# Optimization experiments

Measured on AMD Instinct MI355X. Metric: run time of the kernel, lower is better.

Reference implementation:

```python
import jax, jax.numpy as jnp
import numpy as np

EMBED_DIM = 768
NUM_HEADS = 12
HEAD_DIM = EMBED_DIM // NUM_HEADS
SCALING = HEAD_DIM ** -0.5
B, S = 2, 2048


def setup_inputs() -> dict:
    key = jax.random.key(0)
    k1, k2, k3 = jax.random.split(key, 3)
    x_q = jax.random.normal(k1, (B, S, EMBED_DIM), dtype=jnp.float32)
    # xavier-uniform-ish scaling for weights
    lim_qkv = (6.0 / (EMBED_DIM + 3 * EMBED_DIM)) ** 0.5
    lim_out = (6.0 / (2 * EMBED_DIM)) ** 0.5
    w_qkv = jax.random.uniform(k2, (3 * EMBED_DIM, EMBED_DIM), jnp.float32, -lim_qkv, lim_qkv)
    b_qkv = jnp.zeros((3 * EMBED_DIM,), jnp.float32)
    w_out = jax.random.uniform(k3, (EMBED_DIM, EMBED_DIM), jnp.float32, -lim_out, lim_out)
    b_out = jnp.zeros((EMBED_DIM,), jnp.float32)
    return {"x_q": x_q, "w_qkv": w_qkv, "b_qkv": b_qkv, "w_out": w_out, "b_out": b_out}


def reference(x_q, w_qkv, b_qkv, w_out, b_out):
    b_sz, s_len, _ = x_q.shape
    # qkv projection: (B,S,3E) -> (B,S,3,H,hd) -> split
    qkv = x_q @ w_qkv.T + b_qkv
    qkv = qkv.reshape(b_sz, s_len, 3, NUM_HEADS, HEAD_DIM)
    q = qkv[:, :, 0].transpose(0, 2, 1, 3) * SCALING  # (B,H,S,hd)
    k = qkv[:, :, 1].transpose(0, 2, 1, 3)
    v = qkv[:, :, 2].transpose(0, 2, 1, 3)
    attn = jnp.einsum("bhsd,bhtd->bhst", q, k)  # (B,H,S,S)
    attn = jax.nn.softmax(attn.astype(jnp.float32), axis=-1).astype(attn.dtype)
    out = jnp.einsum("bhst,bhtd->bhsd", attn, v)  # (B,H,S,hd)
    out = out.transpose(0, 2, 1, 3).reshape(b_sz, s_len, EMBED_DIM)
    return out @ w_out.T + b_out
```

## Files before the change

### kernel.cpp

```cpp
#include <hip/hip_runtime.h>
#include <hip/hip_bf16.h>
#include <math.h>

typedef unsigned short u16;
typedef unsigned int u32;
typedef __attribute__((ext_vector_type(8))) short bf16x8;
typedef __attribute__((ext_vector_type(4))) short bf16x4;
typedef __attribute__((ext_vector_type(4))) float f32x4;

#define EMBED 768
#define NHEADS 12
#define HDIM 64
#define NBATCH 2
#define SEQ 2048
#define NTOK 4096
#define QKV_N 2304
#define BHTOT 24
#define QSCALE 0.18033688011112042f

__device__ __forceinline__ u16 f2b(float f) {
    __hip_bfloat16 h = __float2bfloat16(f);
    return __builtin_bit_cast(u16, h);
}
__device__ __forceinline__ u32 pk2(float a, float b) {
    return (u32)f2b(a) | ((u32)f2b(b) << 16);
}
__device__ __forceinline__ f32x4 mfma32(bf16x8 a, bf16x8 b, f32x4 c) {
    return __builtin_amdgcn_mfma_f32_16x16x32_bf16(a, b, c, 0, 0, 0);
}
#if __has_builtin(__builtin_amdgcn_mfma_f32_16x16x16_bf16)
__device__ __forceinline__ f32x4 mfma16(bf16x4 a, bf16x4 b, f32x4 c) {
    return __builtin_amdgcn_mfma_f32_16x16x16_bf16(a, b, c, 0, 0, 0);
}
#else
__device__ __forceinline__ f32x4 mfma16(bf16x4 a, bf16x4 b, f32x4 c) {
    return __builtin_amdgcn_mfma_f32_16x16x16bf16_1k(a, b, c, 0, 0, 0);
}
#endif

__device__ __forceinline__ float exp2_hw(float x) {
#if __has_builtin(__builtin_amdgcn_exp2f)
    return __builtin_amdgcn_exp2f(x);
#else
    float r;
    asm("v_exp_f32 %0, %1" : "=v"(r) : "v"(x));
    return r;
#endif
}

__device__ __forceinline__ void async16(const u16* g, u16* l) {
    __builtin_amdgcn_global_load_lds(
        (const __attribute__((address_space(1))) unsigned int*)g,
        (__attribute__((address_space(3))) unsigned int*)l,
        16, 0, 0);
}

__global__ __launch_bounds__(256)
void cast_kernel(const float* __restrict__ s0, u16* __restrict__ d0, int n0,
                 const float* __restrict__ s1, u16* __restrict__ d1, int n1,
                 const float* __restrict__ s2, u16* __restrict__ d2, int n2)
{
    int idx = (blockIdx.x * 256 + threadIdx.x) * 4;
    const float* s; u16* d; int i;
    if (idx < n0)            { s = s0; d = d0; i = idx; }
    else if (idx < n0 + n1)  { s = s1; d = d1; i = idx - n0; }
    else                     { s = s2; d = d2; i = idx - n0 - n1; if (i >= n2) return; }
    float4 v = *(const float4*)&s[i];
    ushort4 o;
    o.x = f2b(v.x); o.y = f2b(v.y); o.z = f2b(v.z); o.w = f2b(v.w);
    *(ushort4*)&d[i] = o;
}

__global__ __launch_bounds__(256, 3)
void qkv_gemm(const u16* __restrict__ A, const u16* __restrict__ W,
              const float* __restrict__ bias,
              u16* __restrict__ Qb, u16* __restrict__ Kb, u16* __restrict__ VT)
{
    __shared__ __align__(16) u16 smem[24576];
    const int m0 = blockIdx.x * 128;
    const int n0 = blockIdx.y * 128;
    const int tid = threadIdx.x;
    const int w = tid >> 6, l = tid & 63;
    const int c = l & 15, q = l >> 4;
    const int wm = (w >> 1) * 64, wn = (w & 1) * 64;
    const int sr = l >> 2;
    const int gch2 = (l & 3) ^ ((l >> 3) & 3);
    const int NK = EMBED / 32;

#define QSTAGE(KT, BS) {                                                      \
    int k0 = (KT) * 32;                                                       \
    _Pragma("unroll")                                                         \
    for (int j = 0; j < 2; ++j) {                                             \
        int row = j * 64 + w * 16 + sr;                                       \
        int seg = (BS) * 8192 + (j * 64 + w * 16) * 32;                       \
        async16(&A[(size_t)(m0 + row) * EMBED + k0 + gch2 * 8],               \
                &smem[seg + l * 8]);                                          \
        async16(&W[(size_t)(n0 + row) * EMBED + k0 + gch2 * 8],               \
                &smem[seg + 4096 + l * 8]);                                   \
    }                                                                         \
}

    f32x4 acc[4][4] = {};

#define QBODY(KT, BC, BS) {                                                   \
    if ((KT) + 1 < NK) asm volatile("s_waitcnt vmcnt(4)" ::: "memory");       \
    else               asm volatile("s_waitcnt vmcnt(0)" ::: "memory");       \
    __builtin_amdgcn_s_barrier();                                             \
    if ((KT) + 2 < NK) QSTAGE((KT) + 2, BS);                                  \
    const u16* Ab = &smem[(BC) * 8192];                                       \
    const u16* Bb = &smem[(BC) * 8192 + 4096];                                \
    const int cs = (q ^ ((c >> 1) & 3)) << 3;                                 \
    bf16x8 af[4], bfr[4];                                                     \
    _Pragma("unroll")                                                         \
    for (int i = 0; i < 4; ++i)                                               \
        af[i] = *(const bf16x8*)&Ab[(wm + i * 16 + c) * 32 + cs];             \
    _Pragma("unroll")                                                         \
    for (int j = 0; j < 4; ++j)                                               \
        bfr[j] = *(const bf16x8*)&Bb[(wn + j * 16 + c) * 32 + cs];            \
    __builtin_amdgcn_s_setprio(1);                                            \
    _Pragma("unroll")                                                         \
    for (int i = 0; i < 4; ++i)                                               \
        _Pragma("unroll")                                                     \
        for (int j = 0; j < 4; ++j)                                           \
            acc[i][j] = mfma32(af[i], bfr[j], acc[i][j]);                     \
    __builtin_amdgcn_s_setprio(0);                                            \
}

    QSTAGE(0, 0);
    QSTAGE(1, 1);

    for (int kt0 = 0; kt0 < NK; kt0 += 3) {
        QBODY(kt0 + 0, 0, 2);
        QBODY(kt0 + 1, 1, 0);
        QBODY(kt0 + 2, 2, 1);
    }
#undef QSTAGE
#undef QBODY

    const int p = n0 / EMBED;
    const int ncol0 = n0 + wn;
    const int h = (ncol0 % EMBED) / HDIM;
    const int mrow0 = m0 + wm;
    const int b = mrow0 >> 11;
    const int s0 = mrow0 & (SEQ - 1);

    if (p < 2) {
        u16* dst = (p == 0) ? Qb : Kb;
        const float mul = (p == 0) ? QSCALE : 1.0f;
        #pragma unroll
        for (int j = 0; j < 4; ++j) {
            int n = ncol0 + j * 16 + c;
            int d = j * 16 + c;
            float bval = bias[n];
            #pragma unroll
            for (int i = 0; i < 4; ++i) {
                #pragma unroll
                for (int r = 0; r < 4; ++r) {
                    int s = s0 + i * 16 + q * 4 + r;
                    float v = (acc[i][j][r] + bval) * mul;
                    dst[(((size_t)(b * NHEADS + h)) * SEQ + s) * HDIM + d] = f2b(v);
                }
            }
        }
    } else {
        __syncthreads();
        u16* T = smem + w * (64 * 72);
        #pragma unroll
        for (int j = 0; j < 4; ++j) {
            int n = ncol0 + j * 16 + c;
            float bval = bias[n];
            #pragma unroll
            for (int i = 0; i < 4; ++i) {
                uint2 pr;
                pr.x = pk2(acc[i][j][0] + bval, acc[i][j][1] + bval);
                pr.y = pk2(acc[i][j][2] + bval, acc[i][j][3] + bval);
                *(uint2*)&T[(j * 16 + c) * 72 + i * 16 + q * 4] = pr;
            }
        }
        const size_t vtbase = ((size_t)(b * NHEADS + h)) * HDIM * SEQ + s0;
        #pragma unroll
        for (int ii = 0; ii < 8; ++ii) {
            int d = (l >> 3) + 8 * ii;
            int sch = (l & 7) * 8;
            uint4 vv = *(const uint4*)&T[d * 72 + sch];
            *(uint4*)&VT[vtbase + (size_t)d * SEQ + sch] = vv;
        }
    }
}

__global__ __launch_bounds__(256, 3)
void attn_kernel(const u16* __restrict__ Qb, const u16* __restrict__ Kb,
                 const u16* __restrict__ VT, u16* __restrict__ AO)
{
    __shared__ __align__(16) u16 Ks[3][4096];
    __shared__ __align__(16) u16 Vs[3][4096];

    const int blk = blockIdx.x;
    const int g = blk & 7, kk = blk >> 3;
    const int bh = g * 3 + (kk >> 5);
    const int qt = kk & 31;

    const int tid = threadIdx.x;
    const int w = tid >> 6, l = tid & 63;
    const int c = l & 15, q = l >> 4;
    const int wq = w >> 1, wk = w & 1;

    const u16* qg = Qb + ((size_t)bh * SEQ + qt * 64 + wq * 32) * HDIM;
    const u16* kg = Kb + ((size_t)bh * SEQ) * HDIM;
    const u16* vg = VT + ((size_t)bh * HDIM) * SEQ;

    const int r8 = l >> 3, ch = l & 7;
    const int gch = ch ^ r8;

    bf16x8 bq[2][2];
    #pragma unroll
    for (int qb2 = 0; qb2 < 2; ++qb2) {
        bq[qb2][0] = *(const bf16x8*)&qg[(qb2 * 16 + c) * HDIM + q * 8];
        bq[qb2][1] = *(const bf16x8*)&qg[(qb2 * 16 + c) * HDIM + 32 + q * 8];
    }

    f32x4 o[4][2] = {};
    float lrow[2] = {0.f, 0.f};

    const int NT = SEQ / 64;

#define STAGE(JT, BS) {                                                       \
    int row0 = w * 16 + r8;                                                   \
    async16(&kg[(size_t)((JT) * 64 + row0) * HDIM + gch * 8],                 \
            &Ks[BS][(w * 16) * 64 + l * 8]);                                  \
    async16(&vg[(size_t)row0 * SEQ + (JT) * 64 + gch * 8],                    \
            &Vs[BS][(w * 16) * 64 + l * 8]);                                  \
    async16(&kg[(size_t)((JT) * 64 + row0 + 8) * HDIM + gch * 8],             \
            &Ks[BS][(w * 16 + 8) * 64 + l * 8]);                              \
    async16(&vg[(size_t)(row0 + 8) * SEQ + (JT) * 64 + gch * 8],              \
            &Vs[BS][(w * 16 + 8) * 64 + l * 8]);                              \
}

#define QKT(SN, BN) {                                                         \
    __builtin_amdgcn_s_setprio(1);                                            \
    _Pragma("unroll")                                                         \
    for (int kb2 = 0; kb2 < 2; ++kb2) {                                       \
        bf16x8 ak0 = *(const bf16x8*)&Ks[BN][(wk * 32 + kb2 * 16 + c) * 64 +  \
                                             (((q    ) ^ (c & 7)) << 3)];     \
        bf16x8 ak1 = *(const bf16x8*)&Ks[BN][(wk * 32 + kb2 * 16 + c) * 64 +  \
                                             (((q | 4) ^ (c & 7)) << 3)];     \
        _Pragma("unroll")                                                     \
        for (int qb2 = 0; qb2 < 2; ++qb2) {                                   \
            f32x4 zz = {};                                                    \
            zz = mfma32(ak0, bq[qb2][0], zz);                                 \
            SN[kb2][qb2] = mfma32(ak1, bq[qb2][1], zz);                       \
        }                                                                     \
    }                                                                         \
    __builtin_amdgcn_s_setprio(0);                                            \
}

#define SOFTPV(SC, BC) {                                                      \
    _Pragma("unroll")                                                         \
    for (int kb2 = 0; kb2 < 2; ++kb2)                                         \
        _Pragma("unroll")                                                     \
        for (int qb2 = 0; qb2 < 2; ++qb2) {                                   \
            float p0 = exp2_hw(SC[kb2][qb2][0]);                              \
            float p1 = exp2_hw(SC[kb2][qb2][1]);                              \
            float p2 = exp2_hw(SC[kb2][qb2][2]);                              \
            float p3 = exp2_hw(SC[kb2][qb2][3]);                              \
            SC[kb2][qb2][0] = p0; SC[kb2][qb2][1] = p1;                       \
            SC[kb2][qb2][2] = p2; SC[kb2][qb2][3] = p3;                       \
            lrow[qb2] += (p0 + p1) + (p2 + p3);                               \
        }                                                                     \
    bf16x4 bp[2][2];                                                          \
    _Pragma("unroll")                                                         \
    for (int kb2 = 0; kb2 < 2; ++kb2)                                         \
        _Pragma("unroll")                                                     \
        for (int qb2 = 0; qb2 < 2; ++qb2) {                                   \
            uint2 pr;                                                         \
            pr.x = pk2(SC[kb2][qb2][0], SC[kb2][qb2][1]);                     \
            pr.y = pk2(SC[kb2][qb2][2], SC[kb2][qb2][3]);                     \
            bp[kb2][qb2] = __builtin_bit_cast(bf16x4, pr);                    \
        }                                                                     \
    __builtin_amdgcn_s_setprio(1);                                            \
    _Pragma("unroll")                                                         \
    for (int db = 0; db < 4; ++db) {                                          \
        bf16x4 av0 = *(const bf16x4*)&Vs[BC][(db * 16 + c) * 64 +             \
                  (((4 * wk     + (q >> 1)) ^ (c & 7)) << 3) + ((q & 1) << 2)]; \
        bf16x4 av1 = *(const bf16x4*)&Vs[BC][(db * 16 + c) * 64 +             \
                  (((4 * wk + 2 + (q >> 1)) ^ (c & 7)) << 3) + ((q & 1) << 2)]; \
        _Pragma("unroll")                                                     \
        for (int qb2 = 0; qb2 < 2; ++qb2) {                                   \
            o[db][qb2] = mfma16(av0, bp[0][qb2], o[db][qb2]);                 \
            o[db][qb2] = mfma16(av1, bp[1][qb2], o[db][qb2]);                 \
        }                                                                     \
    }                                                                         \
    __builtin_amdgcn_s_setprio(0);                                            \
}

#define BODY(J, SC, SN, BC, BN, BS) {                                         \
    asm volatile("s_waitcnt vmcnt(0)" ::: "memory");                          \
    __builtin_amdgcn_s_barrier();                                             \
    if ((J) + 2 < NT) STAGE((J) + 2, BS);                                     \
    if ((J) + 1 < NT) QKT(SN, BN);                                            \
    SOFTPV(SC, BC);                                                           \
}

    f32x4 scA[2][2], scB[2][2];

    STAGE(0, 0);
    STAGE(1, 1);
    asm volatile("s_waitcnt vmcnt(4)" ::: "memory");
    __builtin_amdgcn_s_barrier();
    QKT(scA, 0);

    for (int jb = 0; jb < 30; jb += 6) {
        BODY(jb + 0, scA, scB, 0, 1, 2);
        BODY(jb + 1, scB, scA, 1, 2, 0);
        BODY(jb + 2, scA, scB, 2, 0, 1);
        BODY(jb + 3, scB, scA, 0, 1, 2);
        BODY(jb + 4, scA, scB, 1, 2, 0);
        BODY(jb + 5, scB, scA, 2, 0, 1);
    }
    BODY(30, scA, scB, 0, 1, 2);
    SOFTPV(scB, 1);

#undef STAGE
#undef QKT
#undef SOFTPV
#undef BODY

    #pragma unroll
    for (int qb2 = 0; qb2 < 2; ++qb2) {
        lrow[qb2] += __shfl_xor(lrow[qb2], 16);
        lrow[qb2] += __shfl_xor(lrow[qb2], 32);
    }

    __syncthreads();
    float* SCR = (float*)&Ks[0][0];
    float* LR  = SCR + 4096;

    if (wk == 1) {
        #pragma unroll
        for (int db = 0; db < 4; ++db)
            #pragma unroll
            for (int qb2 = 0; qb2 < 2; ++qb2)
                *(f32x4*)&SCR[((wq * 8 + db * 2 + qb2) << 8) + l * 4] = o[db][qb2];
        if (q == 0) {
            LR[(wq * 2 + 0) * 16 + c] = lrow[0];
            LR[(wq * 2 + 1) * 16 + c] = lrow[1];
        }
    }
    __syncthreads();

    if (wk == 0) {
        float inv[2];
        #pragma unroll
        for (int qb2 = 0; qb2 < 2; ++qb2)
            inv[qb2] = 1.0f / (lrow[qb2] + LR[(wq * 2 + qb2) * 16 + c]);
        const int b = bh / NHEADS, h = bh % NHEADS;
        #pragma unroll
        for (int qb2 = 0; qb2 < 2; ++qb2) {
            const int s = qt * 64 + wq * 32 + qb2 * 16 + c;
            u16* ao = AO + ((size_t)(b * SEQ + s)) * EMBED + h * HDIM;
            #pragma unroll
            for (int db = 0; db < 4; ++db) {
                f32x4 part = *(const f32x4*)&SCR[((wq * 8 + db * 2 + qb2) << 8) + l * 4];
                f32x4 t = o[db][qb2] + part;
                uint2 oo;
                oo.x = pk2(t[0] * inv[qb2], t[1] * inv[qb2]);
                oo.y = pk2(t[2] * inv[qb2], t[3] * inv[qb2]);
                *(uint2*)&ao[db * 16 + q * 4] = oo;
            }
        }
    }
}

__global__ __launch_bounds__(256, 3)
void out_gemm(const u16* __restrict__ A, const u16* __restrict__ W,
              const float* __restrict__ bias, float* __restrict__ out)
{
    __shared__ __align__(16) u16 smem[12288];
    const int m0 = blockIdx.x * 64;
    const int n0 = blockIdx.y * 64;
    const int tid = threadIdx.x;
    const int w = tid >> 6, l = tid & 63;
    const int c = l & 15, q = l >> 4;
    const int sr = l >> 2;
    const int gch2 = (l & 3) ^ ((l >> 3) & 3);
    const int NK = EMBED / 32;

#define OSTAGE(KT, BS) {                                                      \
    int k0 = (KT) * 32;                                                       \
    int row = w * 16 + sr;                                                    \
    int seg = (BS) * 4096 + (w * 16) * 32;                                    \
    async16(&A[(size_t)(m0 + row) * EMBED + k0 + gch2 * 8],                   \
            &smem[seg + l * 8]);                                              \
    async16(&W[(size_t)(n0 + row) * EMBED + k0 + gch2 * 8],                   \
            &smem[seg + 2048 + l * 8]);                                       \
}

    f32x4 acc[4] = {};

#define OBODY(KT, BC, BS) {                                                   \
    if ((KT) + 1 < NK) asm volatile("s_waitcnt vmcnt(2)" ::: "memory");       \
    else               asm volatile("s_waitcnt vmcnt(0)" ::: "memory");       \
    __builtin_amdgcn_s_barrier();                                             \
    if ((KT) + 2 < NK) OSTAGE((KT) + 2, BS);                                  \
    const u16* Ab = &smem[(BC) * 4096];                                       \
    const u16* Bb = &smem[(BC) * 4096 + 2048];                                \
    const int cs = (q ^ ((c >> 1) & 3)) << 3;                                 \
    bf16x8 af = *(const bf16x8*)&Ab[(w * 16 + c) * 32 + cs];                  \
    bf16x8 bfr[4];                                                            \
    _Pragma("unroll")                                                         \
    for (int j = 0; j < 4; ++j)                                               \
        bfr[j] = *(const bf16x8*)&Bb[(j * 16 + c) * 32 + cs];                 \
    __builtin_amdgcn_s_setprio(1);                                            \
    _Pragma("unroll")                                                         \
    for (int j = 0; j < 4; ++j)                                               \
        acc[j] = mfma32(af, bfr[j], acc[j]);                                  \
    __builtin_amdgcn_s_setprio(0);                                            \
}

    OSTAGE(0, 0);
    OSTAGE(1, 1);

    for (int kt0 = 0; kt0 < NK; kt0 += 3) {
        OBODY(kt0 + 0, 0, 2);
        OBODY(kt0 + 1, 1, 0);
        OBODY(kt0 + 2, 2, 1);
    }
#undef OSTAGE
#undef OBODY

    #pragma unroll
    for (int j = 0; j < 4; ++j) {
        int n = n0 + j * 16 + c;
        float bval = bias[n];
        #pragma unroll
        for (int r = 0; r < 4; ++r) {
            int m = m0 + w * 16 + q * 4 + r;
            out[(size_t)m * EMBED + n] = acc[j][r] + bval;
        }
    }
}

extern "C" void kernel_launch(void* const* d_in, const int* in_sizes, int n_in,
                              void* d_out, int out_size, void* d_ws, size_t ws_size,
                              hipStream_t stream)
{
    const float* x    = (const float*)d_in[0];
    const float* wqkv = (const float*)d_in[1];
    const float* bqkv = (const float*)d_in[2];
    const float* wout = (const float*)d_in[3];
    const float* bout = (const float*)d_in[4];
    float* out = (float*)d_out;

    const int nx  = NTOK * EMBED;
    const int nwq = QKV_N * EMBED;
    const int nwo = EMBED * EMBED;
    const size_t per = (size_t)NBATCH * NHEADS * SEQ * HDIM;

    u16* xb    = (u16*)d_ws;
    u16* wqkvb = xb + nx;
    u16* woutb = wqkvb + nwq;
    u16* Qb    = woutb + nwo;
    u16* Kb    = Qb + per;
    u16* VT    = Kb + per;
    u16* AO    = VT + per;

    int castTot = (nx + nwq + nwo) / 4;
    cast_kernel<<<castTot / 256, 256, 0, stream>>>(x, xb, nx, wqkv, wqkvb, nwq, wout, woutb, nwo);

    dim3 g1(NTOK / 128, QKV_N / 128);
    qkv_gemm<<<g1, 256, 0, stream>>>(xb, wqkvb, bqkv, Qb, Kb, VT);

    attn_kernel<<<BHTOT * 32, 256, 0, stream>>>(Qb, Kb, VT, AO);

    dim3 g3(NTOK / 64, EMBED / 64);
    out_gemm<<<g3, 256, 0, stream>>>(AO, woutb, bout, out);
}
```

Before: 150.9 us.

## Halve attention query tile to 32 rows, double-buffer K/V, raise occupancy

The attention kernel now handles 32 query rows per block instead of 64 and launches twice as many blocks. The K/V shared-memory ring drops from triple to double buffering, and the software-pipelined QK^T prefetch across iterations is replaced by a simple load-compute loop. Launch bounds rise to 5 waves per SIMD, aiming for more occupancy and better CU coverage. In exchange, each K/V tile is loaded twice as often per query row, and the cross-iteration overlap of QK^T with softmax/PV is lost.

```diff
diff --git a/kernel.cpp b/kernel.cpp
--- a/kernel.cpp
+++ b/kernel.cpp
@@ -188,39 +188,35 @@
     }
 }
 
-__global__ __launch_bounds__(256, 3)
+__global__ __launch_bounds__(256, 5)
 void attn_kernel(const u16* __restrict__ Qb, const u16* __restrict__ Kb,
                  const u16* __restrict__ VT, u16* __restrict__ AO)
 {
-    __shared__ __align__(16) u16 Ks[3][4096];
-    __shared__ __align__(16) u16 Vs[3][4096];
+    __shared__ __align__(16) u16 Ks[2][4096];
+    __shared__ __align__(16) u16 Vs[2][4096];
 
     const int blk = blockIdx.x;
     const int g = blk & 7, kk = blk >> 3;
-    const int bh = g * 3 + (kk >> 5);
-    const int qt = kk & 31;
+    const int bh = g * 3 + (kk >> 6);
+    const int qt = kk & 63;
 
     const int tid = threadIdx.x;
     const int w = tid >> 6, l = tid & 63;
     const int c = l & 15, q = l >> 4;
     const int wq = w >> 1, wk = w & 1;
 
-    const u16* qg = Qb + ((size_t)bh * SEQ + qt * 64 + wq * 32) * HDIM;
+    const u16* qg = Qb + ((size_t)bh * SEQ + qt * 32 + wq * 16) * HDIM;
     const u16* kg = Kb + ((size_t)bh * SEQ) * HDIM;
     const u16* vg = VT + ((size_t)bh * HDIM) * SEQ;
 
     const int r8 = l >> 3, ch = l & 7;
     const int gch = ch ^ r8;
 
-    bf16x8 bq[2][2];
-    #pragma unroll
-    for (int qb2 = 0; qb2 < 2; ++qb2) {
-        bq[qb2][0] = *(const bf16x8*)&qg[(qb2 * 16 + c) * HDIM + q * 8];
-        bq[qb2][1] = *(const bf16x8*)&qg[(qb2 * 16 + c) * HDIM + 32 + q * 8];
-    }
-
-    f32x4 o[4][2] = {};
-    float lrow[2] = {0.f, 0.f};
+    bf16x8 bq0 = *(const bf16x8*)&qg[c * HDIM + q * 8];
+    bf16x8 bq1 = *(const bf16x8*)&qg[c * HDIM + 32 + q * 8];
+
+    f32x4 o[4] = {};
+    float lrow = 0.f;
 
     const int NT = SEQ / 64;
 
@@ -228,55 +224,52 @@
     int row0 = w * 16 + r8;                                                   \
     async16(&kg[(size_t)((JT) * 64 + row0) * HDIM + gch * 8],                 \
             &Ks[BS][(w * 16) * 64 + l * 8]);                                  \
+    async16(&kg[(size_t)((JT) * 64 + row0 + 8) * HDIM + gch * 8],             \
+            &Ks[BS][(w * 16 + 8) * 64 + l * 8]);                              \
     async16(&vg[(size_t)row0 * SEQ + (JT) * 64 + gch * 8],                    \
             &Vs[BS][(w * 16) * 64 + l * 8]);                                  \
-    async16(&kg[(size_t)((JT) * 64 + row0 + 8) * HDIM + gch * 8],             \
-            &Ks[BS][(w * 16 + 8) * 64 + l * 8]);                              \
     async16(&vg[(size_t)(row0 + 8) * SEQ + (JT) * 64 + gch * 8],              \
             &Vs[BS][(w * 16 + 8) * 64 + l * 8]);                              \
 }
 
-#define QKT(SN, BN) {                                                         \
-    __builtin_amdgcn_s_setprio(1);                                            \
-    _Pragma("unroll")                                                         \
-    for (int kb2 = 0; kb2 < 2; ++kb2) {                                       \
-        bf16x8 ak0 = *(const bf16x8*)&Ks[BN][(wk * 32 + kb2 * 16 + c) * 64 +  \
+#define BODY(J, BC) {                                                         \
+    asm volatile("s_waitcnt vmcnt(0)" ::: "memory");                          \
+    __builtin_amdgcn_s_barrier();                                             \
+    if ((J) + 1 < NT) STAGE((J) + 1, (BC) ^ 1);                               \
+         \
+    f32x4 sc0, sc1;                                                           \
+    {                                                                         \
+        bf16x8 ak0 = *(const bf16x8*)&Ks[BC][(wk * 32 + c) * 64 +             \
                                              (((q    ) ^ (c & 7)) << 3)];     \
-        bf16x8 ak1 = *(const bf16x8*)&Ks[BN][(wk * 32 + kb2 * 16 + c) * 64 +  \
+        bf16x8 ak1 = *(const bf16x8*)&Ks[BC][(wk * 32 + c) * 64 +             \
                                              (((q | 4) ^ (c & 7)) << 3)];     \
-        _Pragma("unroll")                                                     \
-        for (int qb2 = 0; qb2 < 2; ++qb2) {                                   \
-            f32x4 zz = {};                                                    \
-            zz = mfma32(ak0, bq[qb2][0], zz);                                 \
-            SN[kb2][qb2] = mfma32(ak1, bq[qb2][1], zz);                       \
-        }                                                                     \
+        bf16x8 bk0 = *(const bf16x8*)&Ks[BC][(wk * 32 + 16 + c) * 64 +        \
+                                             (((q    ) ^ (c & 7)) << 3)];     \
+        bf16x8 bk1 = *(const bf16x8*)&Ks[BC][(wk * 32 + 16 + c) * 64 +        \
+                                             (((q | 4) ^ (c & 7)) << 3)];     \
+        __builtin_amdgcn_s_setprio(1);                                        \
+        f32x4 z0 = {}, z1 = {};                                               \
+        z0 = mfma32(ak0, bq0, z0);                                            \
+        sc0 = mfma32(ak1, bq1, z0);                                           \
+        z1 = mfma32(bk0, bq0, z1);                                            \
+        sc1 = mfma32(bk1, bq1, z1);                                           \
+        __builtin_amdgcn_s_setprio(0);                                        \
     }                                                                         \
-    __builtin_amdgcn_s_setprio(0);                                            \
-}
-
-#define SOFTPV(SC, BC) {                                                      \
-    _Pragma("unroll")                                                         \
-    for (int kb2 = 0; kb2 < 2; ++kb2)                                         \
-        _Pragma("unroll")                                                     \
-        for (int qb2 = 0; qb2 < 2; ++qb2) {                                   \
-            float p0 = exp2_hw(SC[kb2][qb2][0]);                              \
-            float p1 = exp2_hw(SC[kb2][qb2][1]);                              \
-            float p2 = exp2_hw(SC[kb2][qb2][2]);                              \
-            float p3 = exp2_hw(SC[kb2][qb2][3]);                              \
-            SC[kb2][qb2][0] = p0; SC[kb2][qb2][1] = p1;                       \
-            SC[kb2][qb2][2] = p2; SC[kb2][qb2][3] = p3;                       \
-            lrow[qb2] += (p0 + p1) + (p2 + p3);                               \
-        }                                                                     \
-    bf16x4 bp[2][2];                                                          \
-    _Pragma("unroll")                                                         \
-    for (int kb2 = 0; kb2 < 2; ++kb2)                                         \
-        _Pragma("unroll")                                                     \
-        for (int qb2 = 0; qb2 < 2; ++qb2) {                                   \
-            uint2 pr;                                                         \
-            pr.x = pk2(SC[kb2][qb2][0], SC[kb2][qb2][1]);                     \
-            pr.y = pk2(SC[kb2][qb2][2], SC[kb2][qb2][3]);                     \
-            bp[kb2][qb2] = __builtin_bit_cast(bf16x4, pr);                    \
-        }                                                                     \
+                    \
+    bf16x4 bp0, bp1;                                                          \
+    {                                                                         \
+        float p0 = exp2_hw(sc0[0]), p1 = exp2_hw(sc0[1]);                     \
+        float p2 = exp2_hw(sc0[2]), p3 = exp2_hw(sc0[3]);                     \
+        float p4 = exp2_hw(sc1[0]), p5 = exp2_hw(sc1[1]);                     \
+        float p6 = exp2_hw(sc1[2]), p7 = exp2_hw(sc1[3]);                     \
+        lrow += ((p0 + p1) + (p2 + p3)) + ((p4 + p5) + (p6 + p7));            \
+        uint2 pr0, pr1;                                                       \
+        pr0.x = pk2(p0, p1); pr0.y = pk2(p2, p3);                             \
+        pr1.x = pk2(p4, p5); pr1.y = pk2(p6, p7);                             \
+        bp0 = __builtin_bit_cast(bf16x4, pr0);                                \
+        bp1 = __builtin_bit_cast(bf16x4, pr1);                                \
+    }                                                                         \
+                 \
     __builtin_amdgcn_s_setprio(1);                                            \
     _Pragma("unroll")                                                         \
     for (int db = 0; db < 4; ++db) {                                          \
@@ -284,89 +277,51 @@
                   (((4 * wk     + (q >> 1)) ^ (c & 7)) << 3) + ((q & 1) << 2)]; \
         bf16x4 av1 = *(const bf16x4*)&Vs[BC][(db * 16 + c) * 64 +             \
                   (((4 * wk + 2 + (q >> 1)) ^ (c & 7)) << 3) + ((q & 1) << 2)]; \
-        _Pragma("unroll")                                                     \
-        for (int qb2 = 0; qb2 < 2; ++qb2) {                                   \
-            o[db][qb2] = mfma16(av0, bp[0][qb2], o[db][qb2]);                 \
-            o[db][qb2] = mfma16(av1, bp[1][qb2], o[db][qb2]);                 \
-        }                                                                     \
+        f32x4 t = o[db];                                                      \
+        t = mfma16(av0, bp0, t);                                              \
+        t = mfma16(av1, bp1, t);                                              \
+        o[db] = t;                                                            \
     }                                                                         \
     __builtin_amdgcn_s_setprio(0);                                            \
 }
 
-#define BODY(J, SC, SN, BC, BN, BS) {                                         \
-    asm volatile("s_waitcnt vmcnt(0)" ::: "memory");                          \
-    __builtin_amdgcn_s_barrier();                                             \
-    if ((J) + 2 < NT) STAGE((J) + 2, BS);                                     \
-    if ((J) + 1 < NT) QKT(SN, BN);                                            \
-    SOFTPV(SC, BC);                                                           \
-}
-
-    f32x4 scA[2][2], scB[2][2];
-
     STAGE(0, 0);
-    STAGE(1, 1);
-    asm volatile("s_waitcnt vmcnt(4)" ::: "memory");
-    __builtin_amdgcn_s_barrier();
-    QKT(scA, 0);
-
-    for (int jb = 0; jb < 30; jb += 6) {
-        BODY(jb + 0, scA, scB, 0, 1, 2);
-        BODY(jb + 1, scB, scA, 1, 2, 0);
-        BODY(jb + 2, scA, scB, 2, 0, 1);
-        BODY(jb + 3, scB, scA, 0, 1, 2);
-        BODY(jb + 4, scA, scB, 1, 2, 0);
-        BODY(jb + 5, scB, scA, 2, 0, 1);
-    }
-    BODY(30, scA, scB, 0, 1, 2);
-    SOFTPV(scB, 1);
-
+
+    for (int j2 = 0; j2 < NT; j2 += 2) {
+        BODY(j2 + 0, 0);
+        BODY(j2 + 1, 1);
+    }
 #undef STAGE
-#undef QKT
-#undef SOFTPV
 #undef BODY
 
-    #pragma unroll
-    for (int qb2 = 0; qb2 < 2; ++qb2) {
-        lrow[qb2] += __shfl_xor(lrow[qb2], 16);
-        lrow[qb2] += __shfl_xor(lrow[qb2], 32);
-    }
+    lrow += __shfl_xor(lrow, 16);
+    lrow += __shfl_xor(lrow, 32);
 
     __syncthreads();
     float* SCR = (float*)&Ks[0][0];
-    float* LR  = SCR + 4096;
+    float* LR  = SCR + 2048;
 
     if (wk == 1) {
         #pragma unroll
         for (int db = 0; db < 4; ++db)
-            #pragma unroll
-            for (int qb2 = 0; qb2 < 2; ++qb2)
-                *(f32x4*)&SCR[((wq * 8 + db * 2 + qb2) << 8) + l * 4] = o[db][qb2];
-        if (q == 0) {
-            LR[(wq * 2 + 0) * 16 + c] = lrow[0];
-            LR[(wq * 2 + 1) * 16 + c] = lrow[1];
-        }
+            *(f32x4*)&SCR[((wq * 4 + db) << 8) + l * 4] = o[db];
+        if (q == 0) LR[wq * 16 + c] = lrow;
     }
     __syncthreads();
 
     if (wk == 0) {
-        float inv[2];
-        #pragma unroll
-        for (int qb2 = 0; qb2 < 2; ++qb2)
-            inv[qb2] = 1.0f / (lrow[qb2] + LR[(wq * 2 + qb2) * 16 + c]);
+        float inv = 1.0f / (lrow + LR[wq * 16 + c]);
         const int b = bh / NHEADS, h = bh % NHEADS;
-        #pragma unroll
-        for (int qb2 = 0; qb2 < 2; ++qb2) {
-            const int s = qt * 64 + wq * 32 + qb2 * 16 + c;
-            u16* ao = AO + ((size_t)(b * SEQ + s)) * EMBED + h * HDIM;
-            #pragma unroll
-            for (int db = 0; db < 4; ++db) {
-                f32x4 part = *(const f32x4*)&SCR[((wq * 8 + db * 2 + qb2) << 8) + l * 4];
-                f32x4 t = o[db][qb2] + part;
-                uint2 oo;
-                oo.x = pk2(t[0] * inv[qb2], t[1] * inv[qb2]);
-                oo.y = pk2(t[2] * inv[qb2], t[3] * inv[qb2]);
-                *(uint2*)&ao[db * 16 + q * 4] = oo;
-            }
+        const int s = qt * 32 + wq * 16 + c;
+        u16* ao = AO + ((size_t)(b * SEQ + s)) * EMBED + h * HDIM;
+        #pragma unroll
+        for (int db = 0; db < 4; ++db) {
+            f32x4 part = *(const f32x4*)&SCR[((wq * 4 + db) << 8) + l * 4];
+            f32x4 t = o[db] + part;
+            uint2 oo;
+            oo.x = pk2(t[0] * inv, t[1] * inv);
+            oo.y = pk2(t[2] * inv, t[3] * inv);
+            *(uint2*)&ao[db * 16 + q * 4] = oo;
         }
     }
 }
@@ -470,7 +425,7 @@
     dim3 g1(NTOK / 128, QKV_N / 128);
     qkv_gemm<<<g1, 256, 0, stream>>>(xb, wqkvb, bqkv, Qb, Kb, VT);
 
-    attn_kernel<<<BHTOT * 32, 256, 0, stream>>>(Qb, Kb, VT, AO);
+    attn_kernel<<<BHTOT * 64, 256, 0, stream>>>(Qb, Kb, VT, AO);
 
     dim3 g3(NTOK / 64, EMBED / 64);
     out_gemm<<<g3, 256, 0, stream>>>(AO, woutb, bout, out);
```

New measurement: 166.1 us. 10.0% more time.

## Fuse fp32-to-bf16 casts into GEMM loads and drop separate cast kernel

Applied to the files above, without the earlier changes.

Removes the standalone cast kernel and instead has qkv_gemm and out_gemm load fp32 inputs and weights into registers, convert them to bf16, and write them to shared memory. The pipeline moves from a 3-stage async global-to-LDS scheme to a 2-buffer register-staged scheme with __syncthreads. This saves one launch and the round trip of writing and rereading the bf16 copies. In exchange the GEMMs read twice the bytes, redo the weight conversion in every tile, and lose the direct async LDS loads, which may hurt their latency hiding.

```diff
diff --git a/kernel.cpp b/kernel.cpp
--- a/kernel.cpp
+++ b/kernel.cpp
@@ -55,28 +55,12 @@
         16, 0, 0);
 }
 
-__global__ __launch_bounds__(256)
-void cast_kernel(const float* __restrict__ s0, u16* __restrict__ d0, int n0,
-                 const float* __restrict__ s1, u16* __restrict__ d1, int n1,
-                 const float* __restrict__ s2, u16* __restrict__ d2, int n2)
-{
-    int idx = (blockIdx.x * 256 + threadIdx.x) * 4;
-    const float* s; u16* d; int i;
-    if (idx < n0)            { s = s0; d = d0; i = idx; }
-    else if (idx < n0 + n1)  { s = s1; d = d1; i = idx - n0; }
-    else                     { s = s2; d = d2; i = idx - n0 - n1; if (i >= n2) return; }
-    float4 v = *(const float4*)&s[i];
-    ushort4 o;
-    o.x = f2b(v.x); o.y = f2b(v.y); o.z = f2b(v.z); o.w = f2b(v.w);
-    *(ushort4*)&d[i] = o;
-}
-
 __global__ __launch_bounds__(256, 3)
-void qkv_gemm(const u16* __restrict__ A, const u16* __restrict__ W,
+void qkv_gemm(const float* __restrict__ A, const float* __restrict__ W,
               const float* __restrict__ bias,
               u16* __restrict__ Qb, u16* __restrict__ Kb, u16* __restrict__ VT)
 {
-    __shared__ __align__(16) u16 smem[24576];
+    __shared__ __align__(16) u16 smem[18432];
     const int m0 = blockIdx.x * 128;
     const int n0 = blockIdx.y * 128;
     const int tid = threadIdx.x;
@@ -84,29 +68,43 @@
     const int c = l & 15, q = l >> 4;
     const int wm = (w >> 1) * 64, wn = (w & 1) * 64;
     const int sr = l >> 2;
-    const int gch2 = (l & 3) ^ ((l >> 3) & 3);
+    const int chs = ((l & 3) ^ ((l >> 3) & 3)) * 8;
     const int NK = EMBED / 32;
 
-#define QSTAGE(KT, BS) {                                                      \
+    float4 ra[2][2], rb[2][2];
+
+#define QLOAD(KT) {                                                           \
     int k0 = (KT) * 32;                                                       \
     _Pragma("unroll")                                                         \
     for (int j = 0; j < 2; ++j) {                                             \
         int row = j * 64 + w * 16 + sr;                                       \
-        int seg = (BS) * 8192 + (j * 64 + w * 16) * 32;                       \
-        async16(&A[(size_t)(m0 + row) * EMBED + k0 + gch2 * 8],               \
-                &smem[seg + l * 8]);                                          \
-        async16(&W[(size_t)(n0 + row) * EMBED + k0 + gch2 * 8],               \
-                &smem[seg + 4096 + l * 8]);                                   \
+        const float* pa = &A[(size_t)(m0 + row) * EMBED + k0 + (l & 3) * 8];  \
+        const float* pb = &W[(size_t)(n0 + row) * EMBED + k0 + (l & 3) * 8];  \
+        ra[j][0] = *(const float4*)pa; ra[j][1] = *(const float4*)(pa + 4);   \
+        rb[j][0] = *(const float4*)pb; rb[j][1] = *(const float4*)(pb + 4);   \
     }                                                                         \
 }
 
+#define QWRITE(BS) {                                                          \
+    _Pragma("unroll")                                                         \
+    for (int j = 0; j < 2; ++j) {                                             \
+        int row = j * 64 + w * 16 + sr;                                       \
+        uint4 pa, pb;                                                         \
+        pa.x = pk2(ra[j][0].x, ra[j][0].y); pa.y = pk2(ra[j][0].z, ra[j][0].w); \
+        pa.z = pk2(ra[j][1].x, ra[j][1].y); pa.w = pk2(ra[j][1].z, ra[j][1].w); \
+        pb.x = pk2(rb[j][0].x, rb[j][0].y); pb.y = pk2(rb[j][0].z, rb[j][0].w); \
+        pb.z = pk2(rb[j][1].x, rb[j][1].y); pb.w = pk2(rb[j][1].z, rb[j][1].w); \
+        *(uint4*)&smem[(BS) * 8192 + row * 32 + chs] = pa;                    \
+        *(uint4*)&smem[(BS) * 8192 + 4096 + row * 32 + chs] = pb;             \
+    }                                                                         \
+}
+
     f32x4 acc[4][4] = {};
 
-#define QBODY(KT, BC, BS) {                                                   \
-    if ((KT) + 1 < NK) asm volatile("s_waitcnt vmcnt(4)" ::: "memory");       \
-    else               asm volatile("s_waitcnt vmcnt(0)" ::: "memory");       \
-    __builtin_amdgcn_s_barrier();                                             \
-    if ((KT) + 2 < NK) QSTAGE((KT) + 2, BS);                                  \
+#define QBODY(KT, BC) {                                                       \
+    __syncthreads();           \
+    if ((KT) + 1 < NK) QWRITE((BC) ^ 1);                                      \
+    if ((KT) + 2 < NK) QLOAD((KT) + 2);                                       \
     const u16* Ab = &smem[(BC) * 8192];                                       \
     const u16* Bb = &smem[(BC) * 8192 + 4096];                                \
     const int cs = (q ^ ((c >> 1) & 3)) << 3;                                 \
@@ -126,15 +124,16 @@
     __builtin_amdgcn_s_setprio(0);                                            \
 }
 
-    QSTAGE(0, 0);
-    QSTAGE(1, 1);
-
-    for (int kt0 = 0; kt0 < NK; kt0 += 3) {
-        QBODY(kt0 + 0, 0, 2);
-        QBODY(kt0 + 1, 1, 0);
-        QBODY(kt0 + 2, 2, 1);
-    }
-#undef QSTAGE
+    QLOAD(0);
+    QWRITE(0);
+    QLOAD(1);
+
+    for (int kt0 = 0; kt0 < NK; kt0 += 2) {
+        QBODY(kt0 + 0, 0);
+        QBODY(kt0 + 1, 1);
+    }
+#undef QLOAD
+#undef QWRITE
 #undef QBODY
 
     const int p = n0 / EMBED;
@@ -371,11 +370,11 @@
     }
 }
 
-__global__ __launch_bounds__(256, 3)
-void out_gemm(const u16* __restrict__ A, const u16* __restrict__ W,
+__global__ __launch_bounds__(256)
+void out_gemm(const u16* __restrict__ A, const float* __restrict__ W,
               const float* __restrict__ bias, float* __restrict__ out)
 {
-    __shared__ __align__(16) u16 smem[12288];
+    __shared__ __align__(16) u16 smem[8192];
     const int m0 = blockIdx.x * 64;
     const int n0 = blockIdx.y * 64;
     const int tid = threadIdx.x;
@@ -383,25 +382,39 @@
     const int c = l & 15, q = l >> 4;
     const int sr = l >> 2;
     const int gch2 = (l & 3) ^ ((l >> 3) & 3);
+    const int chs = gch2 * 8;
     const int NK = EMBED / 32;
 
-#define OSTAGE(KT, BS) {                                                      \
+    float4 rb[2];
+
+#define OBLOAD(KT) {                                                          \
     int k0 = (KT) * 32;                                                       \
     int row = w * 16 + sr;                                                    \
-    int seg = (BS) * 4096 + (w * 16) * 32;                                    \
+    const float* pb = &W[(size_t)(n0 + row) * EMBED + k0 + (l & 3) * 8];      \
+    rb[0] = *(const float4*)pb; rb[1] = *(const float4*)(pb + 4);             \
+}
+
+#define OBWRITE(BS) {                                                         \
+    int row = w * 16 + sr;                                                    \
+    uint4 pb;                                                                 \
+    pb.x = pk2(rb[0].x, rb[0].y); pb.y = pk2(rb[0].z, rb[0].w);               \
+    pb.z = pk2(rb[1].x, rb[1].y); pb.w = pk2(rb[1].z, rb[1].w);               \
+    *(uint4*)&smem[(BS) * 4096 + 2048 + row * 32 + chs] = pb;                 \
+}
+
+#define OAASYNC(KT, BS) {                                                     \
+    int k0 = (KT) * 32;                                                       \
+    int row = w * 16 + sr;                                                    \
     async16(&A[(size_t)(m0 + row) * EMBED + k0 + gch2 * 8],                   \
-            &smem[seg + l * 8]);                                              \
-    async16(&W[(size_t)(n0 + row) * EMBED + k0 + gch2 * 8],                   \
-            &smem[seg + 2048 + l * 8]);                                       \
+            &smem[(BS) * 4096 + (w * 16) * 32 + l * 8]);                      \
 }
 
     f32x4 acc[4] = {};
 
-#define OBODY(KT, BC, BS) {                                                   \
-    if ((KT) + 1 < NK) asm volatile("s_waitcnt vmcnt(2)" ::: "memory");       \
-    else               asm volatile("s_waitcnt vmcnt(0)" ::: "memory");       \
-    __builtin_amdgcn_s_barrier();                                             \
-    if ((KT) + 2 < NK) OSTAGE((KT) + 2, BS);                                  \
+#define OBODY(KT, BC) {                                                       \
+    __syncthreads();     \
+    if ((KT) + 1 < NK) { OBWRITE((BC) ^ 1); OAASYNC((KT) + 1, (BC) ^ 1); }    \
+    if ((KT) + 2 < NK) OBLOAD((KT) + 2);                                      \
     const u16* Ab = &smem[(BC) * 4096];                                       \
     const u16* Bb = &smem[(BC) * 4096 + 2048];                                \
     const int cs = (q ^ ((c >> 1) & 3)) << 3;                                 \
@@ -417,15 +430,18 @@
     __builtin_amdgcn_s_setprio(0);                                            \
 }
 
-    OSTAGE(0, 0);
-    OSTAGE(1, 1);
-
-    for (int kt0 = 0; kt0 < NK; kt0 += 3) {
-        OBODY(kt0 + 0, 0, 2);
-        OBODY(kt0 + 1, 1, 0);
-        OBODY(kt0 + 2, 2, 1);
-    }
-#undef OSTAGE
+    OBLOAD(0);
+    OBWRITE(0);
+    OAASYNC(0, 0);
+    OBLOAD(1);
+
+    for (int kt0 = 0; kt0 < NK; kt0 += 2) {
+        OBODY(kt0 + 0, 0);
+        OBODY(kt0 + 1, 1);
+    }
+#undef OBLOAD
+#undef OBWRITE
+#undef OAASYNC
 #undef OBODY
 
     #pragma unroll
@@ -451,27 +467,18 @@
     const float* bout = (const float*)d_in[4];
     float* out = (float*)d_out;
 
-    const int nx  = NTOK * EMBED;
-    const int nwq = QKV_N * EMBED;
-    const int nwo = EMBED * EMBED;
     const size_t per = (size_t)NBATCH * NHEADS * SEQ * HDIM;
 
-    u16* xb    = (u16*)d_ws;
-    u16* wqkvb = xb + nx;
-    u16* woutb = wqkvb + nwq;
-    u16* Qb    = woutb + nwo;
-    u16* Kb    = Qb + per;
-    u16* VT    = Kb + per;
-    u16* AO    = VT + per;
-
-    int castTot = (nx + nwq + nwo) / 4;
-    cast_kernel<<<castTot / 256, 256, 0, stream>>>(x, xb, nx, wqkv, wqkvb, nwq, wout, woutb, nwo);
+    u16* Qb = (u16*)d_ws;
+    u16* Kb = Qb + per;
+    u16* VT = Kb + per;
+    u16* AO = VT + per;
 
     dim3 g1(NTOK / 128, QKV_N / 128);
-    qkv_gemm<<<g1, 256, 0, stream>>>(xb, wqkvb, bqkv, Qb, Kb, VT);
+    qkv_gemm<<<g1, 256, 0, stream>>>(x, wqkv, bqkv, Qb, Kb, VT);
 
     attn_kernel<<<BHTOT * 32, 256, 0, stream>>>(Qb, Kb, VT, AO);
 
     dim3 g3(NTOK / 64, EMBED / 64);
-    out_gemm<<<g3, 256, 0, stream>>>(AO, woutb, bout, out);
-}
+    out_gemm<<<g3, 256, 0, stream>>>(AO, wout, bout, out);
+}
```

Measured after the change: 159.1 us. 5.5% more time.
